# Performance work log

Measured on AMD Instinct MI355X. Metric: run time of the kernel, lower is better.

Reference implementation:

```python
import jax, jax.numpy as jnp
import numpy as np

L1 = 1536
L2 = 15
L3 = 64
COUNT = 8
B = 16384


def setup_inputs() -> dict:
    key = jax.random.key(0)
    ks = jax.random.split(key, 10)
    d_in = 2 * L1 // 2  # 1536
    s1 = 1.0 / np.sqrt(d_in)
    s2 = 1.0 / np.sqrt(2 * L2)
    s3 = 1.0 / np.sqrt(L3)
    return {
        "x": jax.random.normal(ks[0], (B, d_in), dtype=jnp.float32),
        "ls_indices": jax.random.randint(ks[1], (B,), 0, COUNT, dtype=jnp.int32),
        "W1": jax.random.uniform(ks[2], (COUNT * (L2 + 1), d_in), jnp.float32, -s1, s1),
        "b1": jax.random.uniform(ks[3], (COUNT * (L2 + 1),), jnp.float32, -s1, s1),
        "Wf": jax.random.uniform(ks[4], (L2 + 1, d_in), jnp.float32, -s1, s1),
        "bf": jax.random.uniform(ks[5], (L2 + 1,), jnp.float32, -s1, s1),
        "W2": jax.random.uniform(ks[6], (COUNT * L3, 2 * L2), jnp.float32, -s2, s2),
        "b2": jax.random.uniform(ks[7], (COUNT * L3,), jnp.float32, -s2, s2),
        "Wo": jax.random.uniform(ks[8], (COUNT, L3), jnp.float32, -s3, s3),
        "bo": jax.random.uniform(ks[9], (COUNT,), jnp.float32, -s3, s3),
    }


def reference(x, ls_indices, W1, b1, Wf, bf, W2, b2, Wo, bo):
    count = Wo.shape[0]
    n = x.shape[0]
    idx = ls_indices[:, None, None]  # [B,1,1] selects the per-sample stack

    # l1: all stacks, then gather selected stack row per sample
    l1s = (x @ W1.T + b1).reshape(n, count, L2 + 1)          # [B, count, 16]
    l1f = x @ Wf.T + bf                                       # [B, 16]
    l1c = jnp.take_along_axis(l1s, idx, axis=1)[:, 0]         # [B, 16]

    l1c_, l1c_out = l1c[:, :L2], l1c[:, L2:]                  # [B,15], [B,1]
    l1f_, l1f_out = l1f[:, :L2], l1f[:, L2:]
    l1x = l1c_ + l1f_
    # squared-clipped-ReLU concat: [pow(x,2)*127/128, x] clamped to [0,1]
    l1x = jnp.clip(jnp.concatenate([l1x * l1x * (127.0 / 128.0), l1x], axis=1), 0.0, 1.0)  # [B,30]

    l2s = (l1x @ W2.T + b2).reshape(n, count, L3)             # [B, count, 64]
    l2c = jnp.take_along_axis(l2s, idx, axis=1)[:, 0]         # [B, 64]
    l2x = jnp.clip(l2c, 0.0, 1.0)

    l3s = (l2x @ Wo.T + bo).reshape(n, count, 1)              # [B, count, 1]
    l3c = jnp.take_along_axis(l3s, idx, axis=1)[:, 0]         # [B, 1]
    return l3c + l1f_out + l1c_out
```

## Files before the change

### kernel.cpp

```cpp
#include <hip/hip_runtime.h>
#include <hip/hip_bf16.h>
#include <stdint.h>

#define L1DIM 1536
#define NOUT  144
#define MTILE 64
#define BK    64
#define NITER (L1DIM / BK)
#define NCHUNK16 1152

typedef __bf16 bf16;
typedef __bf16 bf16x8 __attribute__((ext_vector_type(8)));
typedef float  floatx4 __attribute__((ext_vector_type(4)));

__global__ void pack_weights(const float* __restrict__ W1,
                             const float* __restrict__ Wf,
                             bf16* __restrict__ pw) {
    int t = blockIdx.x * blockDim.x + threadIdx.x;
    if (t >= NOUT * 192) return;
    int n = t / 192;
    int o = t % 192;
    const float* src = (n < 128) ? (W1 + (size_t)n * L1DIM + o * 8)
                                 : (Wf + (size_t)(n - 128) * L1DIM + o * 8);
    float4 s0 = ((const float4*)src)[0];
    float4 s1 = ((const float4*)src)[1];
    bf16x8 v;
    v[0] = (bf16)s0.x; v[1] = (bf16)s0.y; v[2] = (bf16)s0.z; v[3] = (bf16)s0.w;
    v[4] = (bf16)s1.x; v[5] = (bf16)s1.y; v[6] = (bf16)s1.z; v[7] = (bf16)s1.w;
    *(bf16x8*)(pw + ((size_t)o * NOUT + n) * 8) = v;
}

__device__ __forceinline__ void gload_lds16(const void* g, void* l) {
    __builtin_amdgcn_global_load_lds(
        (const __attribute__((address_space(1))) void*)g,
        (__attribute__((address_space(3))) void*)l, 16, 0, 0);
}

__global__ __launch_bounds__(512) void layerstacks_main(
    const float* __restrict__ x, const int* __restrict__ lsidx,
    const bf16* __restrict__ pw,
    const float* __restrict__ b1, const float* __restrict__ bf_,
    const float* __restrict__ W2, const float* __restrict__ b2,
    const float* __restrict__ Wo, const float* __restrict__ bo,
    float* __restrict__ out)
{
    __shared__ bf16  lb[2][8 * NOUT * 8];
    __shared__ float ep[MTILE][148];

    const int tid  = threadIdx.x;
    const int wv   = tid >> 6;
    const int ln   = tid & 63;
    const int quad = ln >> 4;
    const int lm   = ln & 15;

    const int R0  = blockIdx.x * MTILE;
    const int rg  = wv & 3;
    const int nh  = wv >> 2;
    const int nt0 = nh ? 5 : 0;
    const int ntn = nh ? 4 : 5;

    const float* xrow = x + (size_t)(R0 + rg * 16 + lm) * L1DIM;

    floatx4 acc[5];
#pragma unroll
    for (int i = 0; i < 5; i++) acc[i] = (floatx4){0.f, 0.f, 0.f, 0.f};

#pragma unroll
    for (int c = 0; c < 3; c++) {
        int ch = tid + c * 512;
        if (ch < NCHUNK16) gload_lds16(pw + (size_t)ch * 8, &lb[0][(size_t)ch * 8]);
    }
    float4 a0 = *(const float4*)(xrow + quad * 8);
    float4 a1 = *(const float4*)(xrow + quad * 8 + 4);
    float4 a2 = *(const float4*)(xrow + 32 + quad * 8);
    float4 a3 = *(const float4*)(xrow + 32 + quad * 8 + 4);
    __syncthreads();

    for (int ki = 0; ki < NITER; ki++) {
        const int cur = ki & 1;
        if (ki < NITER - 1) {
            const bf16* src = pw + (size_t)(ki + 1) * 8 * NOUT * 8;
#pragma unroll
            for (int c = 0; c < 3; c++) {
                int ch = tid + c * 512;
                if (ch < NCHUNK16) gload_lds16(src + (size_t)ch * 8, &lb[cur ^ 1][(size_t)ch * 8]);
            }
        }
        bf16x8 af0, af1;
        af0[0] = (bf16)a0.x; af0[1] = (bf16)a0.y; af0[2] = (bf16)a0.z; af0[3] = (bf16)a0.w;
        af0[4] = (bf16)a1.x; af0[5] = (bf16)a1.y; af0[6] = (bf16)a1.z; af0[7] = (bf16)a1.w;
        af1[0] = (bf16)a2.x; af1[1] = (bf16)a2.y; af1[2] = (bf16)a2.z; af1[3] = (bf16)a2.w;
        af1[4] = (bf16)a3.x; af1[5] = (bf16)a3.y; af1[6] = (bf16)a3.z; af1[7] = (bf16)a3.w;
        if (ki < NITER - 1) {
            const float* xk = xrow + (ki + 1) * BK;
            a0 = *(const float4*)(xk + quad * 8);
            a1 = *(const float4*)(xk + quad * 8 + 4);
            a2 = *(const float4*)(xk + 32 + quad * 8);
            a3 = *(const float4*)(xk + 32 + quad * 8 + 4);
        }
#pragma unroll
        for (int t = 0; t < 5; t++) {
            if (t < ntn) {
                const int nt = nt0 + t;
                bf16x8 bf0 = *(const bf16x8*)&lb[cur][((quad)     * NOUT + nt * 16 + lm) * 8];
                bf16x8 bf1 = *(const bf16x8*)&lb[cur][((4 + quad) * NOUT + nt * 16 + lm) * 8];
                acc[t] = __builtin_amdgcn_mfma_f32_16x16x32_bf16(af0, bf0, acc[t], 0, 0, 0);
                acc[t] = __builtin_amdgcn_mfma_f32_16x16x32_bf16(af1, bf1, acc[t], 0, 0, 0);
            }
        }
        __syncthreads();
    }

#pragma unroll
    for (int t = 0; t < 5; t++) {
        if (t < ntn) {
            const int nt = nt0 + t;
#pragma unroll
            for (int r = 0; r < 4; r++)
                ep[rg * 16 + quad * 4 + r][nt * 16 + lm] = acc[t][r];
        }
    }
    __syncthreads();

    const int er   = tid >> 3;
    const int sub  = tid & 7;
    const int grow = R0 + er;
    const int bkt  = lsidx[grow];

    const float l1c15 = ep[er][bkt * 16 + 15] + b1[bkt * 16 + 15];
    const float l1f15 = ep[er][128 + 15] + bf_[15];

    float l1x[30];
#pragma unroll
    for (int j = 0; j < 15; j++) {
        float tj = (ep[er][bkt * 16 + j] + b1[bkt * 16 + j])
                 + (ep[er][128 + j]      + bf_[j]);
        float sq = tj * tj * (127.0f / 128.0f);
        l1x[j]      = fminf(fmaxf(sq, 0.f), 1.f);
        l1x[15 + j] = fminf(fmaxf(tj, 0.f), 1.f);
    }

    float part = 0.f;
#pragma unroll
    for (int o = 0; o < 8; o++) {
        const int oi = bkt * 64 + sub * 8 + o;
        const float2* wrow = (const float2*)(W2 + oi * 30);
        float a = b2[oi];
#pragma unroll
        for (int j2 = 0; j2 < 15; j2++) {
            float2 w = wrow[j2];
            a += l1x[2 * j2] * w.x + l1x[2 * j2 + 1] * w.y;
        }
        a = fminf(fmaxf(a, 0.f), 1.f);
        part += a * Wo[oi];
    }
    part += __shfl_xor(part, 1);
    part += __shfl_xor(part, 2);
    part += __shfl_xor(part, 4);
    if (sub == 0) out[grow] = part + bo[bkt] + l1c15 + l1f15;
}

extern "C" void kernel_launch(void* const* d_in, const int* in_sizes, int n_in,
                              void* d_out, int out_size, void* d_ws, size_t ws_size,
                              hipStream_t stream) {
    const float* x   = (const float*)d_in[0];
    const int*   idx = (const int*)  d_in[1];
    const float* W1  = (const float*)d_in[2];
    const float* b1  = (const float*)d_in[3];
    const float* Wf  = (const float*)d_in[4];
    const float* bf  = (const float*)d_in[5];
    const float* W2  = (const float*)d_in[6];
    const float* b2  = (const float*)d_in[7];
    const float* Wo  = (const float*)d_in[8];
    const float* bo  = (const float*)d_in[9];
    float* out = (float*)d_out;
    bf16*  pw  = (bf16*)d_ws;

    pack_weights<<<dim3((NOUT * 192 + 255) / 256), dim3(256), 0, stream>>>(W1, Wf, pw);
    layerstacks_main<<<dim3(16384 / MTILE), dim3(512), 0, stream>>>(
        x, idx, pw, b1, bf, W2, b2, Wo, bo, out);
}
```

Baseline: 183.7 us.

## Stage x tiles through LDS with async loads, shrink tile, compact epilogue

Each block now covers 32 rows with 256 threads instead of 64 rows with 512, giving 512 blocks and two blocks per CU through the launch-bounds hint. The x tile is now brought in with global_load_lds into a swizzled, double-buffered LDS array alongside the weights, replacing per-thread register prefetch of x. The epilogue keeps only each row's selected bucket and the shared-path outputs, which shrinks the ep buffer. The goal is better latency hiding and occupancy. In exchange, each block still loads the full weight tile every k-step but for half as many rows, so weight traffic per row doubles.

```diff
diff --git a/kernel.cpp b/kernel.cpp
--- a/kernel.cpp
+++ b/kernel.cpp
@@ -4,10 +4,10 @@
 
 #define L1DIM 1536
 #define NOUT  144
-#define MTILE 64
+#define MTILE 32
 #define BK    64
 #define NITER (L1DIM / BK)
-#define NCHUNK16 1152
+#define BCH   18
 
 typedef __bf16 bf16;
 typedef __bf16 bf16x8 __attribute__((ext_vector_type(8)));
@@ -36,7 +36,14 @@
         (__attribute__((address_space(3))) void*)l, 16, 0, 0);
 }
 
-__global__ __launch_bounds__(512) void layerstacks_main(
+__device__ __forceinline__ bf16x8 cvt8(float4 a, float4 b) {
+    bf16x8 r;
+    r[0] = (bf16)a.x; r[1] = (bf16)a.y; r[2] = (bf16)a.z; r[3] = (bf16)a.w;
+    r[4] = (bf16)b.x; r[5] = (bf16)b.y; r[6] = (bf16)b.z; r[7] = (bf16)b.w;
+    return r;
+}
+
+__global__ __launch_bounds__(256, 2) void layerstacks_main(
     const float* __restrict__ x, const int* __restrict__ lsidx,
     const bf16* __restrict__ pw,
     const float* __restrict__ b1, const float* __restrict__ bf_,
@@ -44,8 +51,9 @@
     const float* __restrict__ Wo, const float* __restrict__ bo,
     float* __restrict__ out)
 {
+    __shared__ float la[2][MTILE * BK];
     __shared__ bf16  lb[2][8 * NOUT * 8];
-    __shared__ float ep[MTILE][148];
+    __shared__ float ep[MTILE][33];
 
     const int tid  = threadIdx.x;
     const int wv   = tid >> 6;
@@ -54,70 +62,81 @@
     const int lm   = ln & 15;
 
     const int R0  = blockIdx.x * MTILE;
-    const int rg  = wv & 3;
-    const int nh  = wv >> 2;
+    const int ms  = wv & 1;
+    const int nh  = wv >> 1;
     const int nt0 = nh ? 5 : 0;
     const int ntn = nh ? 4 : 5;
 
-    const float* xrow = x + (size_t)(R0 + rg * 16 + lm) * L1DIM;
+    const int sr  = ln >> 4;
+    const int sch = ln & 15;
 
     floatx4 acc[5];
 #pragma unroll
     for (int i = 0; i < 5; i++) acc[i] = (floatx4){0.f, 0.f, 0.f, 0.f};
 
-#pragma unroll
-    for (int c = 0; c < 3; c++) {
-        int ch = tid + c * 512;
-        if (ch < NCHUNK16) gload_lds16(pw + (size_t)ch * 8, &lb[0][(size_t)ch * 8]);
-    }
-    float4 a0 = *(const float4*)(xrow + quad * 8);
-    float4 a1 = *(const float4*)(xrow + quad * 8 + 4);
-    float4 a2 = *(const float4*)(xrow + 32 + quad * 8);
-    float4 a3 = *(const float4*)(xrow + 32 + quad * 8 + 4);
+#define STAGE(buf, ki_)                                                          \
+    {                                                                            \
+        const int k0_ = (ki_) * BK;                                              \
+        _Pragma("unroll")                                                        \
+        for (int jj = 0; jj < 2; jj++) {                                         \
+            const int j    = 2 * wv + jj;                                        \
+            const int row  = 4 * j + sr;                                         \
+            const int cg   = sch ^ (row & 7);                                    \
+            gload_lds16(x + (size_t)(R0 + row) * L1DIM + k0_ + cg * 4,           \
+                        &la[buf][j * 4 * BK + sr * BK + sch * 4]);               \
+        }                                                                        \
+        const bf16* bsrc_ = pw + (size_t)(ki_) * 8 * NOUT * 8;                   \
+        _Pragma("unroll")                                                        \
+        for (int cc = wv; cc < BCH; cc += 4) {                                   \
+            gload_lds16(bsrc_ + (size_t)cc * 512 + ln * 8,                       \
+                        &lb[buf][(size_t)cc * 512 + ln * 8]);                    \
+        }                                                                        \
+    }
+
+    STAGE(0, 0)
     __syncthreads();
 
     for (int ki = 0; ki < NITER; ki++) {
         const int cur = ki & 1;
-        if (ki < NITER - 1) {
-            const bf16* src = pw + (size_t)(ki + 1) * 8 * NOUT * 8;
-#pragma unroll
-            for (int c = 0; c < 3; c++) {
-                int ch = tid + c * 512;
-                if (ch < NCHUNK16) gload_lds16(src + (size_t)ch * 8, &lb[cur ^ 1][(size_t)ch * 8]);
-            }
-        }
-        bf16x8 af0, af1;
-        af0[0] = (bf16)a0.x; af0[1] = (bf16)a0.y; af0[2] = (bf16)a0.z; af0[3] = (bf16)a0.w;
-        af0[4] = (bf16)a1.x; af0[5] = (bf16)a1.y; af0[6] = (bf16)a1.z; af0[7] = (bf16)a1.w;
-        af1[0] = (bf16)a2.x; af1[1] = (bf16)a2.y; af1[2] = (bf16)a2.z; af1[3] = (bf16)a2.w;
-        af1[4] = (bf16)a3.x; af1[5] = (bf16)a3.y; af1[6] = (bf16)a3.z; af1[7] = (bf16)a3.w;
-        if (ki < NITER - 1) {
-            const float* xk = xrow + (ki + 1) * BK;
-            a0 = *(const float4*)(xk + quad * 8);
-            a1 = *(const float4*)(xk + quad * 8 + 4);
-            a2 = *(const float4*)(xk + 32 + quad * 8);
-            a3 = *(const float4*)(xk + 32 + quad * 8 + 4);
-        }
-#pragma unroll
-        for (int t = 0; t < 5; t++) {
-            if (t < ntn) {
-                const int nt = nt0 + t;
-                bf16x8 bf0 = *(const bf16x8*)&lb[cur][((quad)     * NOUT + nt * 16 + lm) * 8];
-                bf16x8 bf1 = *(const bf16x8*)&lb[cur][((4 + quad) * NOUT + nt * 16 + lm) * 8];
-                acc[t] = __builtin_amdgcn_mfma_f32_16x16x32_bf16(af0, bf0, acc[t], 0, 0, 0);
-                acc[t] = __builtin_amdgcn_mfma_f32_16x16x32_bf16(af1, bf1, acc[t], 0, 0, 0);
+        if (ki < NITER - 1) STAGE(cur ^ 1, ki + 1)
+
+#pragma unroll
+        for (int s = 0; s < 2; s++) {
+            const int row = ms * 16 + lm;
+            const int c0  = s * 8 + quad * 2;
+            float4 a0 = *(const float4*)&la[cur][row * BK + ((c0)     ^ (row & 7)) * 4];
+            float4 a1 = *(const float4*)&la[cur][row * BK + ((c0 + 1) ^ (row & 7)) * 4];
+            bf16x8 af = cvt8(a0, a1);
+            const bf16* bbase = &lb[cur][((size_t)(s * 4 + quad) * NOUT) * 8];
+#pragma unroll
+            for (int t = 0; t < 5; t++) {
+                if (t < ntn) {
+                    bf16x8 bfrag = *(const bf16x8*)&bbase[((nt0 + t) * 16 + lm) * 8];
+                    acc[t] = __builtin_amdgcn_mfma_f32_16x16x32_bf16(af, bfrag, acc[t], 0, 0, 0);
+                }
             }
         }
         __syncthreads();
     }
 
-#pragma unroll
-    for (int t = 0; t < 5; t++) {
-        if (t < ntn) {
-            const int nt = nt0 + t;
-#pragma unroll
-            for (int r = 0; r < 4; r++)
-                ep[rg * 16 + quad * 4 + r][nt * 16 + lm] = acc[t][r];
+    {
+        const int rbase = ms * 16 + quad * 4;
+#pragma unroll
+        for (int r = 0; r < 4; r++) {
+            const int row = rbase + r;
+            const int bkt = lsidx[R0 + row];
+            if (nh == 0) {
+                float c = acc[0][r];
+#pragma unroll
+                for (int t = 1; t < 5; t++) c = (bkt == t) ? acc[t][r] : c;
+                if (bkt < 5) ep[row][lm] = c;
+            } else {
+                float c = acc[0][r];
+                c = (bkt == 6) ? acc[1][r] : c;
+                c = (bkt == 7) ? acc[2][r] : c;
+                if (bkt >= 5) ep[row][lm] = c;
+                ep[row][16 + lm] = acc[3][r];
+            }
         }
     }
     __syncthreads();
@@ -127,14 +146,13 @@
     const int grow = R0 + er;
     const int bkt  = lsidx[grow];
 
-    const float l1c15 = ep[er][bkt * 16 + 15] + b1[bkt * 16 + 15];
-    const float l1f15 = ep[er][128 + 15] + bf_[15];
+    const float l1c15 = ep[er][15] + b1[bkt * 16 + 15];
+    const float l1f15 = ep[er][31] + bf_[15];
 
     float l1x[30];
 #pragma unroll
     for (int j = 0; j < 15; j++) {
-        float tj = (ep[er][bkt * 16 + j] + b1[bkt * 16 + j])
-                 + (ep[er][128 + j]      + bf_[j]);
+        float tj = (ep[er][j] + b1[bkt * 16 + j]) + (ep[er][16 + j] + bf_[j]);
         float sq = tj * tj * (127.0f / 128.0f);
         l1x[j]      = fminf(fmaxf(sq, 0.f), 1.f);
         l1x[15 + j] = fminf(fmaxf(tj, 0.f), 1.f);
@@ -177,6 +195,6 @@
     bf16*  pw  = (bf16*)d_ws;
 
     pack_weights<<<dim3((NOUT * 192 + 255) / 256), dim3(256), 0, stream>>>(W1, Wf, pw);
-    layerstacks_main<<<dim3(16384 / MTILE), dim3(512), 0, stream>>>(
+    layerstacks_main<<<dim3(16384 / MTILE), dim3(256), 0, stream>>>(
         x, idx, pw, b1, bf, W2, b2, Wo, bo, out);
 }
```

Result: faster. 179.9 us (-2.1%).
